# Kernel tuning notes

Measured on AMD Instinct MI355X. Metric: run time of the kernel, lower is better.

Reference implementation:

```python
import jax, jax.numpy as jnp
import numpy as np

B = 2          # batch
L = 2048       # seq len
D_MODEL = 1024
D_INNER = 2 * D_MODEL   # expand = 2
D_STATE = 16
D_CONV = 4
DT_RANK = D_MODEL // 16  # 64


def setup_inputs() -> dict:
    key = jax.random.key(0)
    kx, kf, kb = jax.random.split(key, 3)
    d = {"x": jax.random.normal(kx, (B, L, D_MODEL), jnp.float32)}
    for pre, k in (("f_", kf), ("b_", kb)):
        kk = jax.random.split(k, 6)
        d[pre + "in_proj_w"] = jax.random.normal(kk[0], (2 * D_INNER, D_MODEL), jnp.float32) * 0.02
        d[pre + "conv_w"] = jax.random.normal(kk[1], (D_INNER, 1, D_CONV), jnp.float32) * 0.2
        d[pre + "conv_b"] = jnp.zeros((D_INNER,), jnp.float32)
        d[pre + "x_proj_w"] = jax.random.normal(kk[2], (DT_RANK + 2 * D_STATE, D_INNER), jnp.float32) * 0.02
        d[pre + "dt_proj_w"] = jax.random.normal(kk[3], (D_INNER, DT_RANK), jnp.float32) * 0.02
        # dt bias init so softplus(bias) ~ dt in [exp(-4), exp(-2)] range (mamba-style)
        d[pre + "dt_proj_b"] = jax.random.uniform(kk[4], (D_INNER,), jnp.float32, minval=-4.0, maxval=-2.0)
        # S4D-real init: A = -[1..d_state]
        d[pre + "A_log"] = jnp.log(jnp.broadcast_to(jnp.arange(1, D_STATE + 1, dtype=jnp.float32), (D_INNER, D_STATE)))
        d[pre + "D"] = jnp.ones((D_INNER,), jnp.float32)
        d[pre + "out_proj_w"] = jax.random.normal(kk[5], (D_MODEL, D_INNER), jnp.float32) * 0.02
    return d


def _silu(x):
    return x * jax.nn.sigmoid(x)


def _selective_scan(u, dt, A, Bm, Cm, Dp):
    # u, dt: [B, L, d_inner]; Bm, Cm: [B, L, d_state]; A: [d_inner, d_state]; Dp: [d_inner]
    def step(h, inp):
        u_t, dt_t, B_t, C_t = inp                       # [B,d], [B,d], [B,n], [B,n]
        dA = jnp.exp(dt_t[..., None] * A)               # [B, d, n]  (ZOH discretization)
        dBu = dt_t[..., None] * B_t[:, None, :] * u_t[..., None]
        h = dA * h + dBu                                # [B, d, n]
        y = jnp.einsum('bdn,bn->bd', h, C_t)            # [B, d]
        return h, y

    h0 = jnp.zeros((u.shape[0], A.shape[0], A.shape[1]), u.dtype)
    xs = (jnp.swapaxes(u, 0, 1), jnp.swapaxes(dt, 0, 1),
          jnp.swapaxes(Bm, 0, 1), jnp.swapaxes(Cm, 0, 1))
    _, ys = jax.lax.scan(step, h0, xs)                  # ys: [L, B, d_inner]
    return jnp.swapaxes(ys, 0, 1) + u * Dp              # skip connection D*u


def _mamba(x, in_proj_w, conv_w, conv_b, x_proj_w, dt_proj_w, dt_proj_b, A_log, Dp, out_proj_w):
    # x: [B, L, d_model]
    xz = x @ in_proj_w.T                                # [B, L, 2*d_inner]
    xi, z = jnp.split(xz, 2, axis=-1)
    # depthwise causal conv1d, kernel D_CONV, output truncated to L (left pad)
    xc = jax.lax.conv_general_dilated(
        jnp.swapaxes(xi, 1, 2), conv_w, (1,), [(D_CONV - 1, 0)],
        dimension_numbers=('NCH', 'OIH', 'NCH'), feature_group_count=D_INNER)
    xi = _silu(jnp.swapaxes(xc, 1, 2) + conv_b)         # [B, L, d_inner]
    x_dbl = xi @ x_proj_w.T                             # [B, L, dt_rank + 2*d_state]
    dt, Bm, Cm = jnp.split(x_dbl, [DT_RANK, DT_RANK + D_STATE], axis=-1)
    dt = jax.nn.softplus(dt @ dt_proj_w.T + dt_proj_b)  # [B, L, d_inner]
    A = -jnp.exp(A_log)                                 # [d_inner, d_state]
    y = _selective_scan(xi, dt, A, Bm, Cm, Dp)
    y = y * _silu(z)                                    # gated
    return y @ out_proj_w.T                             # [B, L, d_model]


def reference(x,
              f_in_proj_w, f_conv_w, f_conv_b, f_x_proj_w, f_dt_proj_w, f_dt_proj_b, f_A_log, f_D, f_out_proj_w,
              b_in_proj_w, b_conv_w, b_conv_b, b_x_proj_w, b_dt_proj_w, b_dt_proj_b, b_A_log, b_D, b_out_proj_w):
    h_fwd = _mamba(x, f_in_proj_w, f_conv_w, f_conv_b, f_x_proj_w,
                   f_dt_proj_w, f_dt_proj_b, f_A_log, f_D, f_out_proj_w)
    h_bwd = _mamba(jnp.flip(x, axis=1), b_in_proj_w, b_conv_w, b_conv_b, b_x_proj_w,
                   b_dt_proj_w, b_dt_proj_b, b_A_log, b_D, b_out_proj_w)
    h_bwd = jnp.flip(h_bwd, axis=1)
    return jnp.concatenate([h_fwd, h_bwd], axis=-1)     # [B, L, 2*d_model]
```

## Files before the change

### kernel.cpp

```cpp
#include <hip/hip_runtime.h>

#define BB 2
#define LL 2048
#define DM 1024
#define DI 2048
#define NTOK (BB*LL)
#define NC 64
#define CL (LL/NC)
#define NCH (BB*DI)

typedef __bf16 bf16x8 __attribute__((ext_vector_type(8)));
typedef float f32x4 __attribute__((ext_vector_type(4)));
typedef int i32x4 __attribute__((ext_vector_type(4)));

#define LOG2E 1.44269504088896340736f

__device__ __forceinline__ float siluf(float x){ return x / (1.f + __expf(-x)); }
__device__ __forceinline__ float softplusf(float x){
  if (x > 20.f) return x;
  return log1pf(__expf(x));
}
__device__ __forceinline__ unsigned short f2bf(float f){
  unsigned int u = __builtin_bit_cast(unsigned int, f);
  u += 0x7fffu + ((u >> 16) & 1u);
  return (unsigned short)(u >> 16);
}
__device__ __forceinline__ float bf2f(unsigned short u){
  return __builtin_bit_cast(float, (unsigned int)u << 16);
}
template<typename CT>
__device__ __forceinline__ void st_ct(CT* p, float v){
  if constexpr (sizeof(CT)==2) *p = (CT)f2bf(v); else *p = (CT)v;
}

__device__ __forceinline__ void gl_lds16(const unsigned short* g, unsigned short* l){
  __builtin_amdgcn_global_load_lds(
      (const __attribute__((address_space(1))) void*)g,
      (__attribute__((address_space(3))) void*)l, 16, 0, 0);
}

#define SEG0 4096
#define SEG1 8192
#define SEG2 512
#define SEG3 256
#define SEG4 4096
#define CAST_BLOCKS (SEG0+SEG1+SEG2+SEG3+SEG4)

__device__ __forceinline__ void cast4(const float* src, unsigned short* dst){
  float4 v = *reinterpret_cast<const float4*>(src);
  ushort4 o; o.x=f2bf(v.x); o.y=f2bf(v.y); o.z=f2bf(v.z); o.w=f2bf(v.w);
  *reinterpret_cast<ushort4*>(dst) = o;
}

__global__ __launch_bounds__(256) void k_cast_all(
    const float* __restrict__ x,
    const float* __restrict__ ipw0, const float* __restrict__ ipw1,
    const float* __restrict__ xpw0, const float* __restrict__ xpw1,
    const float* __restrict__ dtw0, const float* __restrict__ dtw1,
    const float* __restrict__ opw0, const float* __restrict__ opw1,
    unsigned short* __restrict__ x_bf, unsigned short* __restrict__ w_bf,
    unsigned short* __restrict__ wpad, unsigned short* __restrict__ dtw_bf,
    unsigned short* __restrict__ outw){
  int bid = blockIdx.x;
  int ti = threadIdx.x*4;
  if (bid < SEG0){
    int i = bid*1024 + ti;
    cast4(x + i, x_bf + i);
  } else if (bid < SEG0+SEG1){
    int i = (bid-SEG0)*1024 + ti;
    const int n = (2*DI)*DM;
    const float* src = (i < n) ? ipw0 : ipw1;
    int off = (i < n) ? i : i - n;
    cast4(src + off, w_bf + i);
  } else if (bid < SEG0+SEG1+SEG2){
    int i = (bid-SEG0-SEG1)*1024 + ti;
    const int ntotal = 128*DI, nreal = 96*DI;
    int dir = i / ntotal;
    int r = i - dir*ntotal;
    if (r < nreal){
      cast4((dir ? xpw1 : xpw0) + r, wpad + i);
    } else {
      ushort4 z{0,0,0,0};
      *reinterpret_cast<ushort4*>(wpad + i) = z;
    }
  } else if (bid < SEG0+SEG1+SEG2+SEG3){
    int i = (bid-SEG0-SEG1-SEG2)*1024 + ti;
    const int n = DI*64;
    const float* src = (i < n) ? dtw0 : dtw1;
    int off = (i < n) ? i : i - n;
    cast4(src + off, dtw_bf + i);
  } else {
    int i = (bid-SEG0-SEG1-SEG2-SEG3)*1024 + ti;
    const int n = DM*DI;
    const float* src = (i < n) ? opw0 : opw1;
    int off = (i < n) ? i : i - n;
    cast4(src + off, outw + i);
  }
}

template<int NT>
__global__ __launch_bounds__(512) void k_gemm256(
    const unsigned short* __restrict__ A, int lda,
    const unsigned short* __restrict__ Bw, int ldb, long long bz,
    unsigned short* __restrict__ C, unsigned short* __restrict__ C2, int nsplit,
    int ldc, long long cz){
  __shared__ unsigned short L[65536];
  const int dir = blockIdx.z;
  Bw += (size_t)dir*bz;
  const int m0 = blockIdx.y*256;
  const int bn0 = blockIdx.x*256;
  unsigned short* Cout; int n0;
  if (bn0 < nsplit){ Cout = C; n0 = bn0; } else { Cout = C2; n0 = bn0 - nsplit; }
  Cout += (size_t)dir*cz;

  const int tid = threadIdx.x;
  const int w = tid >> 6, lane = tid & 63;
  const int rT = tid >> 2;
  const int sG = (tid & 3) ^ ((tid >> 3) & 3);
  const unsigned short* srcA = A  + (size_t)(m0  + rT)*lda + sG*8;
  const unsigned short* srcB = Bw + (size_t)(bn0 + rT)*ldb + sG*8;
  unsigned short* const lw = &L[w*512];
  const int wmb = (w>>2)*128, wnb = (w&3)*64;
  const int fr = lane & 15;
  const int sk = ((lane>>4) ^ ((fr>>1)&3))*8;

  f32x4 acc[8][4] = {};

  auto STAGE = [&](int kt, int kk, int c){
    const unsigned short* a_ = srcA + kt*64 + kk*32;
    const unsigned short* b_ = srcB + kt*64 + kk*32;
    unsigned short* l_ = lw + c*32768 + kk*16384;
    gl_lds16(a_,                   l_);
    gl_lds16(a_ + (size_t)128*lda, l_ + 4096);
    gl_lds16(b_,                   l_ + 8192);
    gl_lds16(b_ + (size_t)128*ldb, l_ + 12288);
  };

  auto HALF = [&](int c, int kk, bool stage, int kt){
    if (stage) STAGE(kt, kk, c^1);
    const unsigned short* base = &L[c*32768 + kk*16384];
    bf16x8 a[8];
#pragma unroll
    for (int i=0;i<8;i++)
      a[i] = *reinterpret_cast<const bf16x8*>(&base[(wmb + i*16 + fr)*32 + sk]);
    bf16x8 b0 = *reinterpret_cast<const bf16x8*>(&base[8192 + (wnb +  0 + fr)*32 + sk]);
    bf16x8 b1 = *reinterpret_cast<const bf16x8*>(&base[8192 + (wnb + 16 + fr)*32 + sk]);
    __builtin_amdgcn_s_setprio(1);
#pragma unroll
    for (int i=0;i<8;i++){
      acc[i][0] = __builtin_amdgcn_mfma_f32_16x16x32_bf16(a[i], b0, acc[i][0], 0,0,0);
      acc[i][1] = __builtin_amdgcn_mfma_f32_16x16x32_bf16(a[i], b1, acc[i][1], 0,0,0);
    }
    __builtin_amdgcn_s_setprio(0);
    bf16x8 b2 = *reinterpret_cast<const bf16x8*>(&base[8192 + (wnb + 32 + fr)*32 + sk]);
    bf16x8 b3 = *reinterpret_cast<const bf16x8*>(&base[8192 + (wnb + 48 + fr)*32 + sk]);
    __builtin_amdgcn_s_setprio(1);
#pragma unroll
    for (int i=0;i<8;i++){
      acc[i][2] = __builtin_amdgcn_mfma_f32_16x16x32_bf16(a[i], b2, acc[i][2], 0,0,0);
      acc[i][3] = __builtin_amdgcn_mfma_f32_16x16x32_bf16(a[i], b3, acc[i][3], 0,0,0);
    }
    __builtin_amdgcn_s_setprio(0);
  };

  STAGE(0, 0, 0);
  STAGE(0, 1, 0);
#pragma unroll 2
  for (int t = 0; t < NT-1; ++t){
    const int c = t & 1;
    asm volatile("s_waitcnt vmcnt(4)" ::: "memory");
    asm volatile("s_barrier" ::: "memory");
    HALF(c, 0, true, t+1);
    asm volatile("s_waitcnt vmcnt(4)" ::: "memory");
    asm volatile("s_barrier" ::: "memory");
    HALF(c, 1, true, t+1);
  }
  {
    const int c = (NT-1) & 1;
    asm volatile("s_waitcnt vmcnt(4)" ::: "memory");
    asm volatile("s_barrier" ::: "memory");
    HALF(c, 0, false, 0);
    asm volatile("s_waitcnt vmcnt(0)" ::: "memory");
    asm volatile("s_barrier" ::: "memory");
    HALF(c, 1, false, 0);
  }

  const int er = (lane>>4)*4;
#pragma unroll
  for (int i=0;i<8;i++)
#pragma unroll
    for (int j=0;j<4;j++){
      int row = m0 + wmb + i*16 + er;
      int col = n0 + wnb + j*16 + fr;
      unsigned short* cp = Cout + (size_t)row*ldc + col;
#pragma unroll
      for (int r=0;r<4;r++) cp[(size_t)r*ldc] = f2bf(acc[i][j][r]);
    }
}

template<int EPI, int KSPLIT, typename CT>
__global__ __launch_bounds__(256) void k_gemm_bt(
    const unsigned short* __restrict__ A, int lda, long long az,
    const unsigned short* __restrict__ Bw, int ldb, long long bz,
    CT* __restrict__ C, CT* __restrict__ C2, int nsplit,
    int ldc, long long cz, int coffz,
    int K, int coff,
    const float* __restrict__ bias0, const float* __restrict__ bias1){
  __shared__ unsigned short As[128*32];
  __shared__ unsigned short Bs[128*32];
  const int z = blockIdx.z;
  const int dirz = z / KSPLIT, kc = z - dirz*KSPLIT;
  A  += (size_t)dirz*az + (size_t)kc*K;
  Bw += (size_t)dirz*bz + (size_t)kc*K;
  const int bn0 = blockIdx.x*128;
  int n0 = bn0;
  if (bn0 >= nsplit){ C = C2; n0 = bn0 - nsplit; }
  C  += (size_t)z*cz;
  const int co = coff + dirz*coffz;
  const float* bias = dirz ? bias1 : bias0;

  const int t = threadIdx.x;
  const int m0 = blockIdx.y*128;
  const int lane = t & 63, w = t >> 6;
  const int wm = (w>>1)*64, wn = (w&1)*64;

  const int gr = lane >> 2;
  const int gslot = (lane & 3) ^ ((lane >> 3) & 3);
  const unsigned short* gA = A  + (size_t)(m0  + 32*w + gr)*lda + gslot*8;
  const unsigned short* gB = Bw + (size_t)(bn0 + 32*w + gr)*ldb + gslot*8;
  unsigned short* lA = &As[(32*w)*32];
  unsigned short* lB = &Bs[(32*w)*32];

  f32x4 acc[4][4] = {};
  const int fr = lane & 15;
  const int rslot = ((lane>>4) ^ ((lane>>1)&3))*8;

  for (int k0=0; k0<K; k0+=32){
    __syncthreads();
    gl_lds16(gA + k0, lA);
    gl_lds16(gA + (size_t)16*lda + k0, lA + 16*32);
    gl_lds16(gB + k0, lB);
    gl_lds16(gB + (size_t)16*ldb + k0, lB + 16*32);
    __syncthreads();
    bf16x8 af[4], bfr[4];
#pragma unroll
    for (int i=0;i<4;i++){
      af[i]  = *reinterpret_cast<const bf16x8*>(&As[(wm + i*16 + fr)*32 + rslot]);
      bfr[i] = *reinterpret_cast<const bf16x8*>(&Bs[(wn + i*16 + fr)*32 + rslot]);
    }
#pragma unroll
    for (int i=0;i<4;i++)
#pragma unroll
      for (int j=0;j<4;j++)
        acc[i][j] = __builtin_amdgcn_mfma_f32_16x16x32_bf16(af[i], bfr[j], acc[i][j], 0,0,0);
  }
  const int er = (lane>>4)*4;
#pragma unroll
  for (int i=0;i<4;i++)
#pragma unroll
    for (int j=0;j<4;j++){
      int row = m0 + wm + i*16 + er;
      int bcol = n0 + wn + j*16 + fr;
      CT* cp = C + (size_t)row*ldc + co + bcol;
      if (EPI == 1){
        float bv = bias[bcol];
#pragma unroll
        for (int r=0;r<4;r++) st_ct(&cp[(size_t)r*ldc], softplusf(acc[i][j][r] + bv));
      } else {
#pragma unroll
        for (int r=0;r<4;r++) st_ct(&cp[(size_t)r*ldc], acc[i][j][r]);
      }
    }
}

__global__ __launch_bounds__(256) void k_conv_silu(const unsigned short* __restrict__ xpre,
    const float* __restrict__ cw0, const float* __restrict__ cw1,
    const float* __restrict__ cb0, const float* __restrict__ cb1,
    unsigned short* __restrict__ xi_bf){
  const int dir = blockIdx.z;
  const int d0 = threadIdx.x*8;
  const int tok0 = blockIdx.x*4;
  const int b = tok0 >> 11;
  const int t0 = tok0 & (LL-1);
  const float* cw = dir ? cw1 : cw0;
  const float* cb = dir ? cb1 : cb0;
  const unsigned short* xpd = xpre + (size_t)dir*NTOK*DI;
  unsigned short* outp = xi_bf + (size_t)dir*NTOK*DI;

  float wv[4][8];
#pragma unroll
  for (int c=0;c<8;c++){
    float4 w = *reinterpret_cast<const float4*>(cw + (size_t)(d0+c)*4);
    wv[0][c]=w.x; wv[1][c]=w.y; wv[2][c]=w.z; wv[3][c]=w.w;
  }
  float bv[8];
  {
    float4 b0 = *reinterpret_cast<const float4*>(cb + d0);
    float4 b1 = *reinterpret_cast<const float4*>(cb + d0 + 4);
    bv[0]=b0.x; bv[1]=b0.y; bv[2]=b0.z; bv[3]=b0.w;
    bv[4]=b1.x; bv[5]=b1.y; bv[6]=b1.z; bv[7]=b1.w;
  }
  const int rbase = t0 + (dir ? 0 : -3);
  float rows[7][8];
#pragma unroll
  for (int i=0;i<7;i++){
    int r = rbase + i;
    if (r >= 0 && r < LL){
      union { i32x4 v; unsigned short u[8]; } x;
      x.v = *reinterpret_cast<const i32x4*>(xpd + ((size_t)b*LL + r)*DI + d0);
#pragma unroll
      for (int c=0;c<8;c++) rows[i][c] = bf2f(x.u[c]);
    } else {
#pragma unroll
      for (int c=0;c<8;c++) rows[i][c] = 0.f;
    }
  }
#pragma unroll
  for (int j=0;j<4;j++){
    union { i32x4 v; unsigned short u[8]; } o;
#pragma unroll
    for (int c=0;c<8;c++){
      float acc = bv[c];
#pragma unroll
      for (int m=0;m<4;m++){
        float w = dir ? wv[3-m][c] : wv[m][c];
        acc += w * rows[j+m][c];
      }
      o.u[c] = f2bf(siluf(acc));
    }
    *reinterpret_cast<i32x4*>(outp + ((size_t)(tok0+j))*DI + d0) = o.v;
  }
}

__global__ __launch_bounds__(256) void k_xred(const float* __restrict__ part,
    float* __restrict__ xdbl, unsigned short* __restrict__ xdbl_bf){
  int idx = blockIdx.x*256 + threadIdx.x;
  if (idx >= 2*NTOK*96) return;
  int dir = idx / (NTOK*96);
  int rem = idx - dir*(NTOK*96);
  int tok = rem / 96, j = rem - tok*96;
  const float* pd = part + (size_t)dir*4*NTOK*128;
  const size_t czs = (size_t)NTOK*128;
  size_t o = (size_t)tok*128 + j;
  float v = pd[o] + pd[czs + o] + pd[2*czs + o] + pd[3*czs + o];
  xdbl[(size_t)dir*NTOK*96 + (size_t)tok*96 + j] = v;
  if (j < 64) xdbl_bf[(size_t)dir*NTOK*64 + (size_t)tok*64 + j] = f2bf(v);
}

__device__ __forceinline__ void powtree(float q, float* dA){
  dA[0]=q;
  dA[1]=dA[0]*dA[0];
  dA[2]=dA[1]*dA[0];
  dA[3]=dA[1]*dA[1];
  dA[4]=dA[3]*dA[0];
  dA[5]=dA[3]*dA[1];
  dA[6]=dA[3]*dA[2];
  dA[7]=dA[3]*dA[3];
#pragma unroll
  for (int n=8;n<16;n++) dA[n]=dA[7]*dA[n-8];
}
__device__ __forceinline__ bool chk_struct(const float* Alog2){
  bool ok = true;
  float a0 = Alog2[0];
#pragma unroll
  for (int n=1;n<16;n++){
    float e = a0*(float)(n+1);
    ok = ok && (fabsf(Alog2[n]-e) <= 1e-5f*fabsf(e) + 1e-12f);
  }
  return ok;
}

__global__ __launch_bounds__(256) void k_scan_p1(const unsigned short* __restrict__ u,
    const unsigned short* __restrict__ dt, const float* __restrict__ xdbl,
    const float* __restrict__ A_log0, const float* __restrict__ A_log1,
    float* __restrict__ hloc, float* __restrict__ dtsum){
  __shared__ float Bs[CL*16];
  const int dir = blockIdx.z;
  u    += (size_t)dir*NTOK*DI;
  dt   += (size_t)dir*NTOK*DI;
  xdbl += (size_t)dir*NTOK*96;
  const float* A_log = dir ? A_log1 : A_log0;
  const int tid = threadIdx.x;
  const int ch = blockIdx.x*256 + tid;
  const int c = blockIdx.y;
  const int b = (blockIdx.x*256) >> 11;
  const int d = ch & (DI-1);
  for (int i = tid; i < CL*16; i += 256){
    int s = i >> 4, j = i & 15;
    int sg = c*CL + s;
    int tt = dir ? (LL-1-sg) : sg;
    Bs[i] = xdbl[((size_t)b*LL + tt)*96 + 64 + j];
  }
  float Alog2[16];
  {
    const float4* ap = reinterpret_cast<const float4*>(A_log + (size_t)d*16);
#pragma unroll
    for (int q=0;q<4;q++){
      float4 v = ap[q];
      Alog2[q*4+0] = -__expf(v.x)*LOG2E;
      Alog2[q*4+1] = -__expf(v.y)*LOG2E;
      Alog2[q*4+2] = -__expf(v.z)*LOG2E;
      Alog2[q*4+3] = -__expf(v.w)*LOG2E;
    }
  }
  const bool structured = chk_struct(Alog2);
  __syncthreads();
  float h[16];
#pragma unroll
  for (int n=0;n<16;n++) h[n]=0.f;
  float dts = 0.f;
  int tok0 = b*LL + (dir ? (LL-1-c*CL) : c*CL);
  const unsigned short* up = u + (size_t)tok0*DI + d;
  const unsigned short* dtp = dt + (size_t)tok0*DI + d;
  const ptrdiff_t stp = dir ? -(ptrdiff_t)DI : (ptrdiff_t)DI;
  if (structured){
    const float a0 = Alog2[0];
#pragma unroll 2
    for (int s=0; s<CL; s++){
      float uv  = bf2f(*up); up += stp;
      float dtv = bf2f(*dtp); dtp += stp;
      float dtu = dtv*uv;
      dts += dtv;
      const f32x4* br = reinterpret_cast<const f32x4*>(&Bs[s*16]);
      f32x4 B0=br[0], B1=br[1], B2=br[2], B3=br[3];
      float dA[16];
      powtree(__builtin_amdgcn_exp2f(dtv*a0), dA);
#pragma unroll
      for (int n=0;n<16;n++){
        float Bv = (n<4)?B0[n&3] : (n<8)?B1[n&3] : (n<12)?B2[n&3] : B3[n&3];
        h[n] = dA[n]*h[n] + dtu*Bv;
      }
    }
  } else {
#pragma unroll 2
    for (int s=0; s<CL; s++){
      float uv  = bf2f(*up); up += stp;
      float dtv = bf2f(*dtp); dtp += stp;
      float dtu = dtv*uv;
      dts += dtv;
      const f32x4* br = reinterpret_cast<const f32x4*>(&Bs[s*16]);
      f32x4 B0=br[0], B1=br[1], B2=br[2], B3=br[3];
#pragma unroll
      for (int n=0;n<16;n++){
        float dA = __builtin_amdgcn_exp2f(dtv*Alog2[n]);
        float Bv = (n<4)?B0[n&3] : (n<8)?B1[n&3] : (n<12)?B2[n&3] : B3[n&3];
        h[n] = dA*h[n] + dtu*Bv;
      }
    }
  }
  float* hp = hloc + (((size_t)(dir*NC + c)*NCH + ch))*16;
#pragma unroll
  for (int q=0;q<4;q++)
    *reinterpret_cast<f32x4*>(hp + q*4) = f32x4{h[q*4],h[q*4+1],h[q*4+2],h[q*4+3]};
  dtsum[(size_t)(dir*NC + c)*NCH + ch] = dts;
}

__global__ __launch_bounds__(256) void k_scan_comb(float* __restrict__ hloc,
    const float* __restrict__ dtsum,
    const float* __restrict__ A_log0, const float* __restrict__ A_log1){
  int i = blockIdx.x*256 + threadIdx.x;
  int dir = i / (NCH*16);
  int j = i - dir*(NCH*16);
  int ch = j >> 4, n = j & 15;
  int d = ch & (DI-1);
  const float* A_log = dir ? A_log1 : A_log0;
  float Alog2 = -__expf(A_log[(size_t)d*16 + n])*LOG2E;
  float hs = 0.f;
#pragma unroll 4
  for (int c=0; c<NC; c++){
    size_t base = (size_t)(dir*NC + c)*NCH + ch;
    float pa = __builtin_amdgcn_exp2f(dtsum[base]*Alog2);
    size_t idx = base*16 + n;
    float h = hloc[idx];
    hloc[idx] = hs;
    hs = pa*hs + h;
  }
}

__global__ __launch_bounds__(256) void k_scan_p2(unsigned short* __restrict__ uy,
    const unsigned short* __restrict__ dt, const float* __restrict__ xdbl,
    const unsigned short* __restrict__ zbuf,
    const float* __restrict__ A_log0, const float* __restrict__ A_log1,
    const float* __restrict__ Dp0, const float* __restrict__ Dp1,
    const float* __restrict__ hstart){
  __shared__ float BCs[CL*32];
  const int dir = blockIdx.z;
  uy   += (size_t)dir*NTOK*DI;
  dt   += (size_t)dir*NTOK*DI;
  zbuf += (size_t)dir*NTOK*DI;
  xdbl += (size_t)dir*NTOK*96;
  const float* A_log = dir ? A_log1 : A_log0;
  const float* Dp = dir ? Dp1 : Dp0;
  const int tid = threadIdx.x;
  const int ch = blockIdx.x*256 + tid;
  const int c = blockIdx.y;
  const int b = (blockIdx.x*256) >> 11;
  const int d = ch & (DI-1);
  for (int i = tid; i < CL*32; i += 256){
    int s = i >> 5, j = i & 31;
    int sg = c*CL + s;
    int tt = dir ? (LL-1-sg) : sg;
    BCs[i] = xdbl[((size_t)b*LL + tt)*96 + 64 + j];
  }
  float Alog2[16];
  {
    const float4* ap = reinterpret_cast<const float4*>(A_log + (size_t)d*16);
#pragma unroll
    for (int q=0;q<4;q++){
      float4 v = ap[q];
      Alog2[q*4+0] = -__expf(v.x)*LOG2E;
      Alog2[q*4+1] = -__expf(v.y)*LOG2E;
      Alog2[q*4+2] = -__expf(v.z)*LOG2E;
      Alog2[q*4+3] = -__expf(v.w)*LOG2E;
    }
  }
  const bool structured = chk_struct(Alog2);
  float h[16];
  {
    const float* hp = hstart + (((size_t)(dir*NC + c)*NCH + ch))*16;
#pragma unroll
    for (int q=0;q<4;q++){
      f32x4 v = *reinterpret_cast<const f32x4*>(hp + q*4);
      h[q*4]=v[0]; h[q*4+1]=v[1]; h[q*4+2]=v[2]; h[q*4+3]=v[3];
    }
  }
  const float Dval = Dp[d];
  __syncthreads();
  int tok0 = b*LL + (dir ? (LL-1-c*CL) : c*CL);
  unsigned short* up = uy + (size_t)tok0*DI + d;
  const unsigned short* zp = zbuf + (size_t)tok0*DI + d;
  const unsigned short* dtp = dt + (size_t)tok0*DI + d;
  const ptrdiff_t stp = dir ? -(ptrdiff_t)DI : (ptrdiff_t)DI;
  if (structured){
    const float a0 = Alog2[0];
#pragma unroll 2
    for (int s=0; s<CL; s++){
      float uv  = bf2f(*up);
      float zv  = bf2f(*zp); zp += stp;
      float dtv = bf2f(*dtp); dtp += stp;
      float dtu = dtv*uv;
      float y = Dval*uv;
      const f32x4* br = reinterpret_cast<const f32x4*>(&BCs[s*32]);
      f32x4 B0=br[0], B1=br[1], B2=br[2], B3=br[3];
      f32x4 C0=br[4], C1=br[5], C2=br[6], C3=br[7];
      float dA[16];
      powtree(__builtin_amdgcn_exp2f(dtv*a0), dA);
#pragma unroll
      for (int n=0;n<16;n++){
        float Bv = (n<4)?B0[n&3] : (n<8)?B1[n&3] : (n<12)?B2[n&3] : B3[n&3];
        float Cv = (n<4)?C0[n&3] : (n<8)?C1[n&3] : (n<12)?C2[n&3] : C3[n&3];
        h[n] = dA[n]*h[n] + dtu*Bv;
        y += h[n]*Cv;
      }
      *up = f2bf(y * siluf(zv)); up += stp;
    }
  } else {
#pragma unroll 2
    for (int s=0; s<CL; s++){
      float uv  = bf2f(*up);
      float zv  = bf2f(*zp); zp += stp;
      float dtv = bf2f(*dtp); dtp += stp;
      float dtu = dtv*uv;
      float y = Dval*uv;
      const f32x4* br = reinterpret_cast<const f32x4*>(&BCs[s*32]);
      f32x4 B0=br[0], B1=br[1], B2=br[2], B3=br[3];
      f32x4 C0=br[4], C1=br[5], C2=br[6], C3=br[7];
#pragma unroll
      for (int n=0;n<16;n++){
        float dA = __builtin_amdgcn_exp2f(dtv*Alog2[n]);
        float Bv = (n<4)?B0[n&3] : (n<8)?B1[n&3] : (n<12)?B2[n&3] : B3[n&3];
        float Cv = (n<4)?C0[n&3] : (n<8)?C1[n&3] : (n<12)?C2[n&3] : C3[n&3];
        h[n] = dA*h[n] + dtu*Bv;
        y += h[n]*Cv;
      }
      *up = f2bf(y * siluf(zv)); up += stp;
    }
  }
}

extern "C" void kernel_launch(void* const* d_in, const int* in_sizes, int n_in,
                              void* d_out, int out_size, void* d_ws, size_t ws_size,
                              hipStream_t stream){
  (void)in_sizes; (void)n_in; (void)out_size; (void)ws_size;
  const float* x = (const float*)d_in[0];
  const float* ipw[2], *cw[2], *cb[2], *xpw[2], *dtw_[2], *dtb[2], *Alog[2], *Dp[2], *opw[2];
  for (int dir=0; dir<2; dir++){
    ipw[dir]  = (const float*)d_in[1 + dir*9 + 0];
    cw[dir]   = (const float*)d_in[1 + dir*9 + 1];
    cb[dir]   = (const float*)d_in[1 + dir*9 + 2];
    xpw[dir]  = (const float*)d_in[1 + dir*9 + 3];
    dtw_[dir] = (const float*)d_in[1 + dir*9 + 4];
    dtb[dir]  = (const float*)d_in[1 + dir*9 + 5];
    Alog[dir] = (const float*)d_in[1 + dir*9 + 6];
    Dp[dir]   = (const float*)d_in[1 + dir*9 + 7];
    opw[dir]  = (const float*)d_in[1 + dir*9 + 8];
  }
  char* p = (char*)d_ws;
  auto alloc = [&](size_t bytes)->void*{ void* r=(void*)p; p += (bytes+255)&~(size_t)255; return r; };
  unsigned short* x_bf   = (unsigned short*)alloc((size_t)NTOK*DM*2);
  unsigned short* w_bf   = (unsigned short*)alloc((size_t)2*(2*DI)*DM*2);
  float* part            = (float*)w_bf;
  unsigned short* xpre   = (unsigned short*)alloc((size_t)2*NTOK*DI*2);
  unsigned short* zbuf   = (unsigned short*)alloc((size_t)2*NTOK*DI*2);
  unsigned short* xi_bf  = (unsigned short*)alloc((size_t)2*NTOK*DI*2);
  float* xdbl            = (float*)alloc((size_t)2*NTOK*96*4);
  unsigned short* xdbl_bf= (unsigned short*)alloc((size_t)2*NTOK*64*2);
  unsigned short* dt_bf  = (unsigned short*)alloc((size_t)2*NTOK*DI*2);
  unsigned short* wpad   = (unsigned short*)alloc((size_t)2*128*DI*2);
  unsigned short* dtw_bf = (unsigned short*)alloc((size_t)2*DI*64*2);
  unsigned short* outw   = (unsigned short*)alloc((size_t)2*DM*DI*2);
  float* hloc  = (float*)d_ws;
  float* dtsum = (float*)((char*)d_ws + (size_t)32*1024*1024);

  k_cast_all<<<CAST_BLOCKS, 256, 0, stream>>>(
      x, ipw[0], ipw[1], xpw[0], xpw[1], dtw_[0], dtw_[1], opw[0], opw[1],
      x_bf, w_bf, wpad, dtw_bf, outw);

  k_gemm256<16><<<dim3(16,16,2), 512, 0, stream>>>(
      x_bf, DM, w_bf, DM, (long long)(2*DI)*DM,
      xpre, zbuf, DI, DI, (long long)NTOK*DI);
  k_conv_silu<<<dim3(NTOK/4,1,2), 256, 0, stream>>>(xpre, cw[0], cw[1], cb[0], cb[1], xi_bf);
  k_gemm_bt<0,4,float><<<dim3(1,32,8), 256, 0, stream>>>(
      xi_bf, DI, (long long)NTOK*DI, wpad, DI, (long long)128*DI,
      part, part, 1<<30, 128, (long long)NTOK*128, 0, 512, 0, nullptr, nullptr);
  k_xred<<<(2*NTOK*96+255)/256, 256, 0, stream>>>(part, xdbl, xdbl_bf);
  k_gemm_bt<1,1,unsigned short><<<dim3(16,32,2), 256, 0, stream>>>(
      xdbl_bf, 64, (long long)NTOK*64, dtw_bf, 64, (long long)DI*64,
      dt_bf, dt_bf, 1<<30, DI, (long long)NTOK*DI, 0, 64, 0, dtb[0], dtb[1]);
  k_scan_p1<<<dim3(NCH/256, NC, 2), 256, 0, stream>>>(xi_bf, dt_bf, xdbl,
      Alog[0], Alog[1], hloc, dtsum);
  k_scan_comb<<<2*NCH*16/256, 256, 0, stream>>>(hloc, dtsum, Alog[0], Alog[1]);
  k_scan_p2<<<dim3(NCH/256, NC, 2), 256, 0, stream>>>(xi_bf, dt_bf, xdbl, zbuf,
      Alog[0], Alog[1], Dp[0], Dp[1], hloc);
  k_gemm_bt<0,1,float><<<dim3(8,32,2), 256, 0, stream>>>(
      xi_bf, DI, (long long)NTOK*DI, outw, DI, (long long)DM*DI,
      (float*)d_out, (float*)d_out, 1<<30, 2*DM, 0, DM, DI, 0, nullptr, nullptr);
}
```

Before: 374.6 us.

## Generalize the 256-tile GEMM to BN=128 and use it for out_proj

Templates the 512-thread k_gemm256 kernel on output tile width and output type. It adds a 256x128 variant with a direct global-to-LDS double-buffered pipeline and MFMA priority hints. The out_proj GEMM now uses this variant with fp32 output instead of the simpler 128x128 k_gemm_bt kernel. The goal is more data reuse per block and better latency hiding on the out_proj matmul. The trade-off is fewer blocks (256) and a larger LDS footprint, which may limit occupancy.

```diff
diff --git a/kernel.cpp b/kernel.cpp
--- a/kernel.cpp
+++ b/kernel.cpp
@@ -98,18 +98,22 @@
   }
 }
 
-template<int NT>
+template<int NT, int BN, typename CT>
 __global__ __launch_bounds__(512) void k_gemm256(
-    const unsigned short* __restrict__ A, int lda,
+    const unsigned short* __restrict__ A, int lda, long long az,
     const unsigned short* __restrict__ Bw, int ldb, long long bz,
-    unsigned short* __restrict__ C, unsigned short* __restrict__ C2, int nsplit,
+    CT* __restrict__ C, CT* __restrict__ C2, int nsplit,
     int ldc, long long cz){
-  __shared__ unsigned short L[65536];
+  constexpr int KKSH = (BN==256) ? 16384 : 12288;
+  constexpr int BUFSH = 2*KKSH;
+  constexpr int BOFF = (BN==256) ? 8192 : 8192;
+  __shared__ unsigned short L[2*BUFSH];
   const int dir = blockIdx.z;
+  A  += (size_t)dir*az;
   Bw += (size_t)dir*bz;
   const int m0 = blockIdx.y*256;
-  const int bn0 = blockIdx.x*256;
-  unsigned short* Cout; int n0;
+  const int bn0 = blockIdx.x*BN;
+  CT* Cout; int n0;
   if (bn0 < nsplit){ Cout = C; n0 = bn0; } else { Cout = C2; n0 = bn0 - nsplit; }
   Cout += (size_t)dir*cz;
 
@@ -120,31 +124,34 @@
   const unsigned short* srcA = A  + (size_t)(m0  + rT)*lda + sG*8;
   const unsigned short* srcB = Bw + (size_t)(bn0 + rT)*ldb + sG*8;
   unsigned short* const lw = &L[w*512];
-  const int wmb = (w>>2)*128, wnb = (w&3)*64;
+  const int wmb = (w>>2)*128;
+  const int wnb = (BN==256) ? (w&3)*64 : (w&3)*32;
+  constexpr int NJ = (BN==256) ? 4 : 2;
   const int fr = lane & 15;
   const int sk = ((lane>>4) ^ ((fr>>1)&3))*8;
 
-  f32x4 acc[8][4] = {};
+  f32x4 acc[8][NJ] = {};
 
   auto STAGE = [&](int kt, int kk, int c){
     const unsigned short* a_ = srcA + kt*64 + kk*32;
     const unsigned short* b_ = srcB + kt*64 + kk*32;
-    unsigned short* l_ = lw + c*32768 + kk*16384;
+    unsigned short* l_ = lw + c*BUFSH + kk*KKSH;
     gl_lds16(a_,                   l_);
     gl_lds16(a_ + (size_t)128*lda, l_ + 4096);
-    gl_lds16(b_,                   l_ + 8192);
-    gl_lds16(b_ + (size_t)128*ldb, l_ + 12288);
+    gl_lds16(b_,                   l_ + BOFF);
+    if constexpr (BN==256)
+      gl_lds16(b_ + (size_t)128*ldb, l_ + BOFF + 4096);
   };
 
   auto HALF = [&](int c, int kk, bool stage, int kt){
     if (stage) STAGE(kt, kk, c^1);
-    const unsigned short* base = &L[c*32768 + kk*16384];
+    const unsigned short* base = &L[c*BUFSH + kk*KKSH];
     bf16x8 a[8];
 #pragma unroll
     for (int i=0;i<8;i++)
       a[i] = *reinterpret_cast<const bf16x8*>(&base[(wmb + i*16 + fr)*32 + sk]);
-    bf16x8 b0 = *reinterpret_cast<const bf16x8*>(&base[8192 + (wnb +  0 + fr)*32 + sk]);
-    bf16x8 b1 = *reinterpret_cast<const bf16x8*>(&base[8192 + (wnb + 16 + fr)*32 + sk]);
+    bf16x8 b0 = *reinterpret_cast<const bf16x8*>(&base[BOFF + (wnb +  0 + fr)*32 + sk]);
+    bf16x8 b1 = *reinterpret_cast<const bf16x8*>(&base[BOFF + (wnb + 16 + fr)*32 + sk]);
     __builtin_amdgcn_s_setprio(1);
 #pragma unroll
     for (int i=0;i<8;i++){
@@ -152,15 +159,22 @@
       acc[i][1] = __builtin_amdgcn_mfma_f32_16x16x32_bf16(a[i], b1, acc[i][1], 0,0,0);
     }
     __builtin_amdgcn_s_setprio(0);
-    bf16x8 b2 = *reinterpret_cast<const bf16x8*>(&base[8192 + (wnb + 32 + fr)*32 + sk]);
-    bf16x8 b3 = *reinterpret_cast<const bf16x8*>(&base[8192 + (wnb + 48 + fr)*32 + sk]);
-    __builtin_amdgcn_s_setprio(1);
-#pragma unroll
-    for (int i=0;i<8;i++){
-      acc[i][2] = __builtin_amdgcn_mfma_f32_16x16x32_bf16(a[i], b2, acc[i][2], 0,0,0);
-      acc[i][3] = __builtin_amdgcn_mfma_f32_16x16x32_bf16(a[i], b3, acc[i][3], 0,0,0);
-    }
-    __builtin_amdgcn_s_setprio(0);
+    if constexpr (BN==256){
+      bf16x8 b2 = *reinterpret_cast<const bf16x8*>(&base[BOFF + (wnb + 32 + fr)*32 + sk]);
+      bf16x8 b3 = *reinterpret_cast<const bf16x8*>(&base[BOFF + (wnb + 48 + fr)*32 + sk]);
+      __builtin_amdgcn_s_setprio(1);
+#pragma unroll
+      for (int i=0;i<8;i++){
+        acc[i][2] = __builtin_amdgcn_mfma_f32_16x16x32_bf16(a[i], b2, acc[i][2], 0,0,0);
+        acc[i][3] = __builtin_amdgcn_mfma_f32_16x16x32_bf16(a[i], b3, acc[i][3], 0,0,0);
+      }
+      __builtin_amdgcn_s_setprio(0);
+    }
+  };
+
+  auto WAITN = [&](){
+    if constexpr (BN==256) asm volatile("s_waitcnt vmcnt(4)" ::: "memory");
+    else                   asm volatile("s_waitcnt vmcnt(3)" ::: "memory");
   };
 
   STAGE(0, 0, 0);
@@ -168,16 +182,16 @@
 #pragma unroll 2
   for (int t = 0; t < NT-1; ++t){
     const int c = t & 1;
-    asm volatile("s_waitcnt vmcnt(4)" ::: "memory");
+    WAITN();
     asm volatile("s_barrier" ::: "memory");
     HALF(c, 0, true, t+1);
-    asm volatile("s_waitcnt vmcnt(4)" ::: "memory");
+    WAITN();
     asm volatile("s_barrier" ::: "memory");
     HALF(c, 1, true, t+1);
   }
   {
     const int c = (NT-1) & 1;
-    asm volatile("s_waitcnt vmcnt(4)" ::: "memory");
+    WAITN();
     asm volatile("s_barrier" ::: "memory");
     HALF(c, 0, false, 0);
     asm volatile("s_waitcnt vmcnt(0)" ::: "memory");
@@ -189,12 +203,12 @@
 #pragma unroll
   for (int i=0;i<8;i++)
 #pragma unroll
-    for (int j=0;j<4;j++){
+    for (int j=0;j<NJ;j++){
       int row = m0 + wmb + i*16 + er;
       int col = n0 + wnb + j*16 + fr;
-      unsigned short* cp = Cout + (size_t)row*ldc + col;
-#pragma unroll
-      for (int r=0;r<4;r++) cp[(size_t)r*ldc] = f2bf(acc[i][j][r]);
+      CT* cp = Cout + (size_t)row*ldc + col;
+#pragma unroll
+      for (int r=0;r<4;r++) st_ct(&cp[(size_t)r*ldc], acc[i][j][r]);
     }
 }
 
@@ -616,8 +630,8 @@
       x, ipw[0], ipw[1], xpw[0], xpw[1], dtw_[0], dtw_[1], opw[0], opw[1],
       x_bf, w_bf, wpad, dtw_bf, outw);
 
-  k_gemm256<16><<<dim3(16,16,2), 512, 0, stream>>>(
-      x_bf, DM, w_bf, DM, (long long)(2*DI)*DM,
+  k_gemm256<16,256,unsigned short><<<dim3(16,16,2), 512, 0, stream>>>(
+      x_bf, DM, 0, w_bf, DM, (long long)(2*DI)*DM,
       xpre, zbuf, DI, DI, (long long)NTOK*DI);
   k_conv_silu<<<dim3(NTOK/4,1,2), 256, 0, stream>>>(xpre, cw[0], cw[1], cb[0], cb[1], xi_bf);
   k_gemm_bt<0,4,float><<<dim3(1,32,8), 256, 0, stream>>>(
@@ -632,7 +646,7 @@
   k_scan_comb<<<2*NCH*16/256, 256, 0, stream>>>(hloc, dtsum, Alog[0], Alog[1]);
   k_scan_p2<<<dim3(NCH/256, NC, 2), 256, 0, stream>>>(xi_bf, dt_bf, xdbl, zbuf,
       Alog[0], Alog[1], Dp[0], Dp[1], hloc);
-  k_gemm_bt<0,1,float><<<dim3(8,32,2), 256, 0, stream>>>(
+  k_gemm256<32,128,float><<<dim3(8,16,2), 512, 0, stream>>>(
       xi_bf, DI, (long long)NTOK*DI, outw, DI, (long long)DM*DI,
-      (float*)d_out, (float*)d_out, 1<<30, 2*DM, 0, DM, DI, 0, nullptr, nullptr);
-}
+      (float*)d_out, (float*)d_out, 1<<30, 2*DM, (long long)DM);
+}
```

New measurement: 352.4 us. 1.06x faster.
